# Performance work log

Hardware: AMD Instinct MI355X
Metric: run time of the kernel (lower is better)

Reference implementation:

```python
import jax, jax.numpy as jnp
import numpy as np

N_NODES = 50000
N_EDGES = 800000
IN, HID, OUT = 128, 256, 128
BN_EPS = 1e-5

def setup_inputs() -> dict:
    key = jax.random.key(0)
    ks = jax.random.split(key, 16)
    def lin(k, fan_in, shape):
        b = 1.0 / np.sqrt(fan_in)
        return jax.random.uniform(k, shape, jnp.float32, -b, b)
    return {
        "node_feat": jax.random.normal(ks[0], (N_NODES, IN), jnp.float32),
        "coord_feat": jax.random.normal(ks[1], (N_NODES, 3), jnp.float32),
        "src": jax.random.randint(ks[2], (N_EDGES,), 0, N_NODES, jnp.int32),
        "dst": jax.random.randint(ks[3], (N_EDGES,), 0, N_NODES, jnp.int32),
        "W_e1": lin(ks[4], 2 * IN + 1, (2 * IN + 1, HID)),
        "b_e1": jnp.zeros((HID,), jnp.float32),
        "W_e2": lin(ks[5], HID, (HID, HID)),
        "b_e2": jnp.zeros((HID,), jnp.float32),
        "W_c1": lin(ks[6], HID, (HID, HID)),
        "b_c1": jnp.zeros((HID,), jnp.float32),
        "W_c2": lin(ks[7], HID, (HID, 1)),
        "W_n1": lin(ks[8], IN + HID, (IN + HID, HID)),
        "b_n1": jnp.zeros((HID,), jnp.float32),
        "W_n2": lin(ks[9], HID, (HID, OUT)),
        "b_n2": jnp.zeros((OUT,), jnp.float32),
        "gamma": jnp.ones((OUT,), jnp.float32),
        "beta": jnp.zeros((OUT,), jnp.float32),
    }

def reference(node_feat, coord_feat, src, dst, W_e1, b_e1, W_e2, b_e2,
              W_c1, b_c1, W_c2, W_n1, b_n1, W_n2, b_n2, gamma, beta):
    silu = jax.nn.silu
    # per-edge geometry (DGL u_sub_v: src - dst)
    x_diff = coord_feat[src] - coord_feat[dst]              # [E, 3]
    radial = jnp.sum(jnp.square(x_diff), axis=1, keepdims=True)  # [E, 1]
    x_diff = x_diff / (jnp.sqrt(radial) + 1e-30)
    # edge MLP on gathered features
    f = jnp.concatenate([node_feat[src], node_feat[dst], radial], axis=-1)  # [E, 2*IN+1]
    msg_h = silu(silu(f @ W_e1 + b_e1) @ W_e2 + b_e2)       # [E, HID]
    # coord message
    msg_x = (silu(msg_h @ W_c1 + b_c1) @ W_c2) * x_diff     # [E, 3]
    # aggregate at destination nodes
    h_neigh = jax.ops.segment_sum(msg_h, dst, num_segments=N_NODES)  # sum
    x_sum = jax.ops.segment_sum(msg_x, dst, num_segments=N_NODES)
    deg = jax.ops.segment_sum(jnp.ones((msg_x.shape[0],), msg_x.dtype), dst,
                              num_segments=N_NODES)
    x_neigh = x_sum / jnp.maximum(deg, 1.0)[:, None]        # mean; 0 for isolated nodes
    # node MLP + BatchNorm (training-mode batch stats, biased var)
    h = silu(jnp.concatenate([node_feat, h_neigh], axis=-1) @ W_n1 + b_n1) @ W_n2 + b_n2
    mu = jnp.mean(h, axis=0)
    var = jnp.mean(jnp.square(h - mu), axis=0)
    h = (h - mu) * jax.lax.rsqrt(var + BN_EPS) * gamma + beta
    x = coord_feat + x_neigh
    return h, x
```

## Files before the change

kernel.cpp:

```cpp
#include <hip/hip_runtime.h>
#include <stdint.h>

typedef unsigned short u16;
typedef __bf16 bf16x8 __attribute__((ext_vector_type(8)));
typedef unsigned short u16x8 __attribute__((ext_vector_type(8)));
typedef float f32x4 __attribute__((ext_vector_type(4)));

#define N_NODES 50000
#define N_EDGES 800000

enum : uint32_t {
  WS_WT_E1 = 0u,
  WS_WT_E2 = 131072u,
  WS_WT_C1 = 262144u,
  WS_WT_N1 = 393216u,
  WS_WT_N2 = 589824u,
  WS_WRAD  = 655360u,
  WS_WC2   = 656384u,
  WS_B_E1  = 657408u,
  WS_B_E2  = 658432u,
  WS_B_C1  = 659456u,
  WS_B_N1  = 660480u,
  WS_B_N2  = 661504u,
  WS_GAMMA = 662016u,
  WS_BETA  = 662528u,
  WS_SCALE = 663040u,
  WS_SHIFT = 663552u,
  WS_STAT  = 664064u,
  WS_FLAG  = 665600u,
  WS_DEG   = 1048576u,
  WS_OFF   = 1248576u,
  WS_BSUM  = 1448704u,
  WS_BPRE  = 1449728u,
  WS_CUR   = 1450752u,
  WS_EID   = 1650752u,
  WS_XSUM  = 4850752u,
  WS_CF    = 5450752u,
  WS_NF    = 6050752u,
  WS_HN    = 18850752u,
  WS_PA    = 70050752u,
  WS_PB    = 95675328u,
  WS_PRE_END = 121299904u
};

__device__ __forceinline__ float b2f(u16 u){ uint32_t x=((uint32_t)u)<<16; float f; __builtin_memcpy(&f,&x,4); return f; }
__device__ __forceinline__ u16 f2b(float f){ __bf16 h = (__bf16)f; return __builtin_bit_cast(unsigned short, h); }
__device__ __forceinline__ float silu_f(float x){
  return x * __builtin_amdgcn_rcpf(1.0f + __expf(-x));
}
__device__ __forceinline__ float ldin(const void* p, int i, int fl){
  return fl ? ((const float*)p)[i] : b2f(((const u16*)p)[i]);
}

__global__ void detect_k(const void* nf, int* flag){
  if (threadIdx.x == 0){
    const u16* p = (const u16*)nf;
    int cnt = 0;
    for (int i=0;i<128;i++){
      u16 u = p[2*i];
      int e = (u >> 7) & 0xFF;
      if (e >= 0x90) cnt++;
    }
    *flag = (cnt >= 8) ? 1 : 0;
  }
}

__global__ void prep_all_k(const void* nf, const void* cd,
                           const void* We1, const void* be1, const void* We2, const void* be2,
                           const void* Wc1, const void* bc1, const void* Wc2,
                           const void* Wn1, const void* bn1, const void* Wn2, const void* bn2,
                           const void* gam, const void* bet,
                           const int* __restrict__ dst, int* __restrict__ deg,
                           char* ws, const int* flagp)
{
  const int b = blockIdx.x;
  const int fl = *flagp;
  if (b < 6250){
    int i = b*256 + threadIdx.x;
    if (i >= (N_NODES*128)/4) return;
    ushort4* out = (ushort4*)(ws + WS_NF);
    if (fl){
      const float4* p = (const float4*)nf;
      float4 v = p[i];
      ushort4 o; o.x=f2b(v.x); o.y=f2b(v.y); o.z=f2b(v.z); o.w=f2b(v.w);
      out[i] = o;
    } else {
      out[i] = ((const ushort4*)nf)[i];
    }
    return;
  }
  if (b < 6837){
    int i = (b-6250)*256 + threadIdx.x;
    if (i >= N_NODES*3) return;
    ((float*)(ws + WS_CF))[i] = ldin(cd, i, fl);
    return;
  }
  if (b < 8125){
    int g = (b-6837)*256 + threadIdx.x;
    if (g < 65536){ int n=g>>8,k=g&255; ((u16*)(ws+WS_WT_E1))[n*256+k]=f2b(ldin(We1,k*256+n,fl)); return; } g-=65536;
    if (g < 65536){
      int j=g&7, l=(g>>3)&63, nblk=(g>>9)&15, kk=g>>13;
      int n=nblk*16+(l&15), k=kk*32+((l>>4)&3)*8+j;
      ((u16*)(ws+WS_WT_E2))[g]=f2b(ldin(We2,k*256+n,fl)); return; } g-=65536;
    if (g < 65536){
      int j=g&7, l=(g>>3)&63, nblk=(g>>9)&15, kk=g>>13;
      int n=nblk*16+(l&15), k=kk*32+((l>>4)&3)*8+j;
      ((u16*)(ws+WS_WT_C1))[g]=f2b(ldin(Wc1,k*256+n,fl)); return; } g-=65536;
    if (g < 98304){ int n=g/384,k=g-n*384; ((u16*)(ws+WS_WT_N1))[n*384+k]=f2b(ldin(Wn1,k*256+n,fl)); return; } g-=98304;
    if (g < 32768){ int n=g>>8,k=g&255; ((u16*)(ws+WS_WT_N2))[n*256+k]=f2b(ldin(Wn2,k*128+n,fl)); return; } g-=32768;
    if (g < 256){ ((float*)(ws+WS_WRAD))[g]=ldin(We1,65536+g,fl); return; } g-=256;
    if (g < 256){ ((float*)(ws+WS_WC2))[g]=ldin(Wc2,g,fl); return; } g-=256;
    if (g < 256){ ((float*)(ws+WS_B_E1))[g]=ldin(be1,g,fl); return; } g-=256;
    if (g < 256){ ((float*)(ws+WS_B_E2))[g]=ldin(be2,g,fl); return; } g-=256;
    if (g < 256){ ((float*)(ws+WS_B_C1))[g]=ldin(bc1,g,fl); return; } g-=256;
    if (g < 256){ ((float*)(ws+WS_B_N1))[g]=ldin(bn1,g,fl); return; } g-=256;
    if (g < 128){ ((float*)(ws+WS_B_N2))[g]=ldin(bn2,g,fl); return; } g-=128;
    if (g < 128){ ((float*)(ws+WS_GAMMA))[g]=ldin(gam,g,fl); return; } g-=128;
    if (g < 128){ ((float*)(ws+WS_BETA))[g]=ldin(bet,g,fl); return; }
    return;
  }
  {
    int e = (b-8125)*256 + threadIdx.x;
    if (e < N_EDGES) atomicAdd(&deg[dst[e]], 1);
  }
}

__global__ void scanA_k(const int* __restrict__ deg, int* __restrict__ off, int* __restrict__ bsum){
  int t = threadIdx.x; int i = blockIdx.x*256 + t;
  int lane = t & 63, w = t >> 6;
  int v = (i < N_NODES) ? deg[i] : 0;
  int x = v;
  #pragma unroll
  for (int d=1; d<64; d<<=1){ int o = __shfl_up(x, d, 64); if (lane >= d) x += o; }
  __shared__ int wt[4];
  if (lane == 63) wt[w] = x;
  __syncthreads();
  int add = 0;
  if (w > 0) add += wt[0];
  if (w > 1) add += wt[1];
  if (w > 2) add += wt[2];
  x += add;
  if (i < N_NODES) off[i] = x;
  if (t == 255) bsum[blockIdx.x] = x;
}

__global__ void scanB_k(const int* __restrict__ bsum, int* __restrict__ bpre, int* __restrict__ off){
  int t = threadIdx.x;
  int lane = t & 63, w = t >> 6;
  int v = (t < 196) ? bsum[t] : 0;
  int x = v;
  #pragma unroll
  for (int d=1; d<64; d<<=1){ int o = __shfl_up(x, d, 64); if (lane >= d) x += o; }
  __shared__ int wt[4];
  if (lane == 63) wt[w] = x;
  __syncthreads();
  int add = 0;
  if (w > 0) add += wt[0];
  if (w > 1) add += wt[1];
  if (w > 2) add += wt[2];
  x += add;
  if (t < 196) bpre[t] = x - v;
  if (t == 255) off[N_NODES] = x;
}

__global__ void scanC_k(const int* __restrict__ deg, int* __restrict__ off,
                        const int* __restrict__ bpre, int* __restrict__ cur){
  int i = blockIdx.x*256 + threadIdx.x;
  if (i >= N_NODES) return;
  int excl = off[i] - deg[i] + bpre[blockIdx.x];
  off[i] = excl; cur[i] = excl;
}

__global__ void scatter_k(const int* __restrict__ dst, int* __restrict__ cur, int* __restrict__ eid){
  int e = blockIdx.x*256 + threadIdx.x;
  if (e >= N_EDGES) return;
  int p = atomicAdd(&cur[dst[e]], 1);
  eid[p] = e;
}

__global__ __launch_bounds__(512, 4) void pab_k(const u16* __restrict__ nfc,
                                                const char* __restrict__ wsw,
                                                u16* __restrict__ pa, u16* __restrict__ pb)
{
  const int t = threadIdx.x, lane = t & 63, wid = t >> 6;
  const int mw = wid & 1, nw = wid >> 1;
  const int mbase = mw << 5, nbase = nw << 6;
  const int l15 = lane & 15, l4 = lane >> 4;
  const int tile = blockIdx.x;
  const u16* Wt = (const u16*)(wsw + WS_WT_E1);
  const float* b1 = (const float*)(wsw + WS_B_E1);

  for (int sel = 0; sel < 2; ++sel){
    u16* out = sel ? pb : pa;
    f32x4 acc[2][4];
    #pragma unroll
    for (int mi=0;mi<2;mi++)
    #pragma unroll
    for (int ni=0;ni<4;ni++){ float b_ = sel ? 0.f : b1[nbase+ni*16+l15]; acc[mi][ni]=(f32x4){b_,b_,b_,b_}; }

    #pragma unroll
    for (int kk=0;kk<4;kk++){
      const int kel = kk*32 + l4*8;
      bf16x8 av[2];
      #pragma unroll
      for (int mi=0;mi<2;mi++){
        int row = tile*64 + mbase + mi*16 + l15;
        if (row >= N_NODES) row = 0;
        av[mi] = *(const bf16x8*)(nfc + (size_t)row*128 + kel);
      }
      #pragma unroll
      for (int ni=0;ni<4;ni++){
        int n_ = nbase + ni*16 + l15;
        bf16x8 bv = *(const bf16x8*)(Wt + (size_t)n_*256 + sel*128 + kel);
        #pragma unroll
        for (int mi=0;mi<2;mi++)
          acc[mi][ni] = __builtin_amdgcn_mfma_f32_16x16x32_bf16(av[mi], bv, acc[mi][ni], 0,0,0);
      }
    }
    #pragma unroll
    for (int mi=0;mi<2;mi++)
    #pragma unroll
    for (int ni=0;ni<4;ni++)
    #pragma unroll
    for (int j=0;j<4;j++){
      int m_ = tile*64 + mbase + mi*16 + l4*4 + j;
      if (m_ < N_NODES){
        int n_ = nbase + ni*16 + l15;
        out[(size_t)m_*256 + n_] = f2b(acc[mi][ni][j]);
      }
    }
  }
}

#define FRAG_GEMM2(FB, BIAS_L) do { \
  _Pragma("unroll") for (int mi=0;mi<2;mi++) _Pragma("unroll") for (int ni=0;ni<4;ni++){ \
    float b_ = BIAS_L[nbase + ni*16 + l15]; acc[mi][ni] = (f32x4){b_,b_,b_,b_}; } \
  bf16x8 bvc[4]; \
  _Pragma("unroll") for (int ni=0;ni<4;ni++) \
    bvc[ni] = *(const bf16x8*)(FB + (((nblk0 + ni)<<9)) + lane*8); \
  _Pragma("unroll") for (int kk=0;kk<8;kk++){ \
    const int kel = kk*32 + l4*8; \
    bf16x8 av[2]; \
    _Pragma("unroll") for (int mi=0;mi<2;mi++){ \
      int row = mbase + mi*16 + l15; \
      uint32_t byte = ((uint32_t)row<<9) ^ ((uint32_t)kel<<1) ^ ((uint32_t)(row&7)<<4); \
      av[mi] = *(const bf16x8*)((const char*)h_lds + byte); \
    } \
    bf16x8 bvn[4]; \
    if (kk < 7){ \
      _Pragma("unroll") for (int ni=0;ni<4;ni++) \
        bvn[ni] = *(const bf16x8*)(FB + ((((kk+1)<<4) + nblk0 + ni)<<9) + lane*8); \
    } \
    _Pragma("unroll") for (int ni=0;ni<4;ni++) \
    _Pragma("unroll") for (int mi=0;mi<2;mi++) \
      acc[mi][ni] = __builtin_amdgcn_mfma_f32_16x16x32_bf16(av[mi], bvc[ni], acc[mi][ni], 0,0,0); \
    if (kk < 7){ \
      _Pragma("unroll") for (int ni=0;ni<4;ni++) bvc[ni] = bvn[ni]; \
    } \
  } } while(0)

#define SILU_STORE2() do { \
  _Pragma("unroll") for (int mi=0;mi<2;mi++) _Pragma("unroll") for (int ni=0;ni<4;ni++) \
  _Pragma("unroll") for (int j=0;j<4;j++){ \
    int m_ = mbase + mi*16 + l4*4 + j; int n_ = nbase + ni*16 + l15; \
    float v_ = silu_f(acc[mi][ni][j]); \
    uint32_t byte = ((uint32_t)m_<<9) ^ ((uint32_t)n_<<1) ^ ((uint32_t)(m_&7)<<4); \
    *(u16*)((char*)h_lds + byte) = f2b(v_); \
  } } while(0)

template<bool PRE>
__global__ __launch_bounds__(512, 4) void edge_mlp(
    const u16* __restrict__ nfc, const float* __restrict__ coord,
    const int* __restrict__ src, const int* __restrict__ dst,
    const char* __restrict__ wsw, const int* __restrict__ eid,
    const u16* __restrict__ pa, const u16* __restrict__ pb,
    float* __restrict__ h_neigh, float* __restrict__ xsum)
{
  __shared__ u16 h_lds[16384];
  __shared__ int s_ids[64], d_ids[64];
  __shared__ float rad_l[64], xd_l[64][3];
  __shared__ float cpart[4][64];
  __shared__ float b1_l[256], b2_l[256], b3_l[256], wc2_l[256];

  const int t = threadIdx.x, lane = t & 63, wid = t >> 6;
  const int mw = wid & 1, nw = wid >> 1;
  const int mbase = mw << 5, nbase = nw << 6;
  const int nblk0 = nw << 2;
  const int l15 = lane & 15, l4 = lane >> 4;

  const int orig = blockIdx.x;
  const int xcd = orig & 7;
  const int tile = (xcd < 4 ? xcd*1563 : 4*1563 + (xcd-4)*1562) + (orig >> 3);

  const u16* FB2 = (const u16*)(wsw + WS_WT_E2);
  const u16* FB3 = (const u16*)(wsw + WS_WT_C1);

  if (t < 64) {
    int e = eid[tile*64 + t];
    int s = src[e], d = dst[e];
    s_ids[t] = s; d_ids[t] = d;
    float ax = coord[s*3+0]-coord[d*3+0];
    float ay = coord[s*3+1]-coord[d*3+1];
    float az = coord[s*3+2]-coord[d*3+2];
    float r2 = ax*ax+ay*ay+az*az;
    float inv = 1.0f/(sqrtf(r2) + 1e-30f);
    rad_l[t] = r2; xd_l[t][0]=ax*inv; xd_l[t][1]=ay*inv; xd_l[t][2]=az*inv;
  }
  if (t >= 64 && t < 320) {
    int c = t - 64;
    if constexpr (!PRE) b1_l[c] = ((const float*)(wsw+WS_B_E1))[c];
    b2_l[c]  = ((const float*)(wsw+WS_B_E2))[c];
    b3_l[c]  = ((const float*)(wsw+WS_B_C1))[c];
    wc2_l[c] = ((const float*)(wsw+WS_WC2))[c];
  }
  __syncthreads();

  f32x4 acc[2][4];

  if constexpr (PRE) {
    const int r1 = t >> 3, cq = (t & 7) << 5;
    const int s1 = s_ids[r1], d1 = d_ids[r1];
    const float rr = rad_l[r1];
    const u16* par = pa + (size_t)s1*256 + cq;
    const u16* pbr = pb + (size_t)d1*256 + cq;
    const float* wrg = (const float*)(wsw + WS_WRAD) + cq;
    u16x8 ua[4], ub[4];
    #pragma unroll
    for (int q=0;q<4;q++){ ua[q] = *(const u16x8*)(par + q*8); ub[q] = *(const u16x8*)(pbr + q*8); }
    #pragma unroll
    for (int q=0;q<4;q++){
      f32x4 w0 = *(const f32x4*)(wrg + q*8);
      f32x4 w1 = *(const f32x4*)(wrg + q*8 + 4);
      u16x8 o;
      #pragma unroll
      for (int j=0;j<8;j++){
        float wv = (j<4) ? w0[j] : w1[j-4];
        float hv = silu_f(b2f(ua[q][j]) + b2f(ub[q][j]) + rr*wv);
        o[j] = f2b(hv);
      }
      int c = cq + q*8;
      uint32_t byte = ((uint32_t)r1<<9) ^ ((uint32_t)c<<1) ^ ((uint32_t)(r1&7)<<4);
      *(u16x8*)((char*)h_lds + byte) = o;
    }
  } else {
    #pragma unroll
    for (int mi=0;mi<2;mi++)
    #pragma unroll
    for (int ni=0;ni<4;ni++){ float b_ = b1_l[nbase+ni*16+l15]; acc[mi][ni]=(f32x4){b_,b_,b_,b_}; }
    const u16* Wt1 = (const u16*)(wsw + WS_WT_E1);
    #pragma unroll
    for (int kk=0;kk<8;kk++){
      const int kel = kk*32 + l4*8;
      bf16x8 av[2];
      #pragma unroll
      for (int mi=0;mi<2;mi++){
        int row = mbase + mi*16 + l15;
        int nid = (kk < 4) ? s_ids[row] : d_ids[row];
        int k = (kk < 4) ? kel : (kel - 128);
        av[mi] = *(const bf16x8*)(nfc + (size_t)nid*128 + k);
      }
      #pragma unroll
      for (int ni=0;ni<4;ni++){
        int n_ = nbase + ni*16 + l15;
        bf16x8 bv = *(const bf16x8*)(Wt1 + (size_t)n_*256 + kel);
        #pragma unroll
        for (int mi=0;mi<2;mi++)
          acc[mi][ni] = __builtin_amdgcn_mfma_f32_16x16x32_bf16(av[mi], bv, acc[mi][ni], 0,0,0);
      }
    }
    #pragma unroll
    for (int mi=0;mi<2;mi++)
    #pragma unroll
    for (int ni=0;ni<4;ni++){
      int n_ = nbase + ni*16 + l15;
      float wrn = ((const float*)(wsw+WS_WRAD))[n_];
      #pragma unroll
      for (int j=0;j<4;j++){
        int m_ = mbase + mi*16 + l4*4 + j;
        float v_ = silu_f(acc[mi][ni][j] + rad_l[m_]*wrn);
        uint32_t byte = ((uint32_t)m_<<9) ^ ((uint32_t)n_<<1) ^ ((uint32_t)(m_&7)<<4);
        *(u16*)((char*)h_lds + byte) = f2b(v_);
      }
    }
  }
  __syncthreads();

  FRAG_GEMM2(FB2, b2_l);
  __syncthreads();
  SILU_STORE2();
  __syncthreads();

  FRAG_GEMM2(FB3, b3_l);
  float part[2][4];
  #pragma unroll
  for (int mi=0;mi<2;mi++)
  #pragma unroll
  for (int j=0;j<4;j++) part[mi][j] = 0.f;
  #pragma unroll
  for (int mi=0;mi<2;mi++)
  #pragma unroll
  for (int ni=0;ni<4;ni++){
    int n_ = nbase + ni*16 + l15;
    float w = wc2_l[n_];
    #pragma unroll
    for (int j=0;j<4;j++) part[mi][j] += silu_f(acc[mi][ni][j]) * w;
  }
  #pragma unroll
  for (int off_=1; off_<16; off_<<=1)
  #pragma unroll
  for (int mi=0;mi<2;mi++)
  #pragma unroll
  for (int j=0;j<4;j++) part[mi][j] += __shfl_xor(part[mi][j], off_, 64);
  if (l15 == 0){
    #pragma unroll
    for (int mi=0;mi<2;mi++)
    #pragma unroll
    for (int j=0;j<4;j++){
      int m_ = mbase + mi*16 + l4*4 + j;
      cpart[nw][m_] = part[mi][j];
    }
  }
  __syncthreads();

  if (t < 64){
    float csum = cpart[0][t] + cpart[1][t] + cpart[2][t] + cpart[3][t];
    int dd = d_ids[t];
    float v0 = csum*xd_l[t][0], v1 = csum*xd_l[t][1], v2 = csum*xd_l[t][2];
    #pragma unroll
    for (int off_=1; off_<64; off_<<=1){
      float u0=__shfl_up(v0,off_,64), u1=__shfl_up(v1,off_,64), u2=__shfl_up(v2,off_,64);
      int du=__shfl_up(dd,off_,64);
      if (lane >= off_ && du == dd){ v0+=u0; v1+=u1; v2+=u2; }
    }
    int dn = __shfl_down(dd,1,64);
    if (lane == 63 || dn != dd){
      unsafeAtomicAdd(&xsum[dd*3+0], v0);
      unsafeAtomicAdd(&xsum[dd*3+1], v1);
      unsafeAtomicAdd(&xsum[dd*3+2], v2);
    }
  }
  {
    int col  = t & 255;
    int half = t >> 8;
    int rb   = half << 5;
    float a2 = 0.f; int prev = d_ids[rb]; bool firstrun = true;
    #pragma unroll
    for (int ii=0; ii<32; ii+=8){
      float v[8]; int dv[8];
      #pragma unroll
      for (int j=0;j<8;j++){
        int m_ = rb + ii + j;
        uint32_t byte = ((uint32_t)m_<<9) ^ ((uint32_t)col<<1) ^ ((uint32_t)(m_&7)<<4);
        v[j] = b2f(*(const u16*)((const char*)h_lds + byte));
        dv[j] = d_ids[m_];
      }
      #pragma unroll
      for (int j=0;j<8;j++){
        if (dv[j] != prev){
          float* p = &h_neigh[(size_t)prev*256 + col];
          if (firstrun) unsafeAtomicAdd(p, a2); else *p = a2;
          firstrun = false; a2 = v[j]; prev = dv[j];
        } else a2 += v[j];
      }
    }
    unsafeAtomicAdd(&h_neigh[(size_t)prev*256 + col], a2);
  }
}

#define SILU_STORE2N() do { \
  _Pragma("unroll") for (int mi=0;mi<2;mi++) _Pragma("unroll") for (int ni=0;ni<4;ni++) \
  _Pragma("unroll") for (int j=0;j<4;j++){ \
    int m_ = mbase + mi*16 + l4*4 + j; int n_ = nbase + ni*16 + l15; \
    float v_ = silu_f(acc[mi][ni][j]); \
    uint32_t byte = ((uint32_t)m_<<9) ^ ((uint32_t)n_<<1) ^ ((uint32_t)(m_&7)<<4); \
    *(u16*)((char*)h_lds + byte) = f2b(v_); \
  } } while(0)

__global__ __launch_bounds__(512, 4) void node_mlp(
    const u16* __restrict__ node_feat, const float* __restrict__ h_neigh,
    const char* __restrict__ wsw, u16* __restrict__ hpre)
{
  __shared__ u16 h_lds[16384];
  __shared__ float b1_l[256], b2_l[128];

  const int t = threadIdx.x, lane = t & 63, wid = t >> 6;
  const int mw = wid & 1, nw = wid >> 1;
  const int mbase = mw << 5, nbase = nw << 6;
  const int l15 = lane & 15, l4 = lane >> 4;
  const int tile = blockIdx.x;

  if (t < 256) b1_l[t] = ((const float*)(wsw+WS_B_N1))[t];
  if (t < 128) b2_l[t] = ((const float*)(wsw+WS_B_N2))[t];
  __syncthreads();

  const u16* Wt1 = (const u16*)(wsw + WS_WT_N1);
  const u16* Wt2 = (const u16*)(wsw + WS_WT_N2);

  f32x4 acc[2][4];
  #pragma unroll
  for (int mi=0;mi<2;mi++)
  #pragma unroll
  for (int ni=0;ni<4;ni++){ float b_ = b1_l[nbase+ni*16+l15]; acc[mi][ni] = (f32x4){b_,b_,b_,b_}; }

  #pragma unroll
  for (int kk=0;kk<12;kk++){
    const int kel = kk*32 + l4*8;
    bf16x8 av[2];
    #pragma unroll
    for (int mi=0;mi<2;mi++){
      int row = tile*64 + mbase + mi*16 + l15;
      if (row >= N_NODES) row = 0;
      if (kk < 4){
        av[mi] = *(const bf16x8*)(node_feat + (size_t)row*128 + kel);
      } else {
        const float* hp = h_neigh + (size_t)row*256 + (kel - 128);
        f32x4 h0 = *(const f32x4*)(hp);
        f32x4 h1 = *(const f32x4*)(hp + 4);
        u16x8 u;
        #pragma unroll
        for (int e2=0;e2<4;e2++){ u[e2] = f2b(h0[e2]); u[e2+4] = f2b(h1[e2]); }
        av[mi] = __builtin_bit_cast(bf16x8, u);
      }
    }
    #pragma unroll
    for (int ni=0;ni<4;ni++){
      int n_ = nbase + ni*16 + l15;
      bf16x8 bv = *(const bf16x8*)(Wt1 + (size_t)n_*384 + kel);
      #pragma unroll
      for (int mi=0;mi<2;mi++)
        acc[mi][ni] = __builtin_amdgcn_mfma_f32_16x16x32_bf16(av[mi], bv, acc[mi][ni], 0,0,0);
    }
  }
  SILU_STORE2N();
  __syncthreads();

  const int nb2 = nw << 5;
  f32x4 acc2[2][2];
  #pragma unroll
  for (int mi=0;mi<2;mi++)
  #pragma unroll
  for (int ni=0;ni<2;ni++){ float b_ = b2_l[nb2+ni*16+l15]; acc2[mi][ni] = (f32x4){b_,b_,b_,b_}; }
  #pragma unroll
  for (int kk=0;kk<8;kk++){
    const int kel = kk*32 + l4*8;
    bf16x8 av[2];
    #pragma unroll
    for (int mi=0;mi<2;mi++){
      int row = mbase + mi*16 + l15;
      uint32_t byte = ((uint32_t)row<<9) ^ ((uint32_t)kel<<1) ^ ((uint32_t)(row&7)<<4);
      av[mi] = *(const bf16x8*)((const char*)h_lds + byte);
    }
    #pragma unroll
    for (int ni=0;ni<2;ni++){
      int n_ = nb2 + ni*16 + l15;
      bf16x8 bv = *(const bf16x8*)(Wt2 + (size_t)n_*256 + kel);
      #pragma unroll
      for (int mi=0;mi<2;mi++)
        acc2[mi][ni] = __builtin_amdgcn_mfma_f32_16x16x32_bf16(av[mi], bv, acc2[mi][ni], 0,0,0);
    }
  }
  #pragma unroll
  for (int mi=0;mi<2;mi++)
  #pragma unroll
  for (int ni=0;ni<2;ni++)
  #pragma unroll
  for (int j=0;j<4;j++){
    int m_ = tile*64 + mbase + mi*16 + l4*4 + j;
    if (m_ < N_NODES){
      int n_ = nb2 + ni*16 + l15;
      hpre[(size_t)m_*128 + n_] = f2b(acc2[mi][ni][j]);
    }
  }
}

__global__ void bn_stats_k(const u16* __restrict__ hpre, float* __restrict__ stat){
  int c = threadIdx.x;
  float s = 0.f, s2 = 0.f;
  for (int r = blockIdx.x; r < N_NODES; r += 256){
    float v = b2f(hpre[(size_t)r*128 + c]);
    s += v; s2 += v*v;
  }
  atomicAdd(&stat[c], s);
  atomicAdd(&stat[128+c], s2);
}

__global__ void bn_final_k(const float* __restrict__ stat, const char* __restrict__ wsw,
                           float* __restrict__ scale, float* __restrict__ shift){
  int c = threadIdx.x;
  if (c >= 128) return;
  float mu = stat[c] * (1.0f/N_NODES);
  float var = stat[128+c] * (1.0f/N_NODES) - mu*mu;
  float rs = rsqrtf(var + 1e-5f);
  float g = ((const float*)(wsw+WS_GAMMA))[c];
  float b = ((const float*)(wsw+WS_BETA))[c];
  scale[c] = rs*g;
  shift[c] = b - mu*rs*g;
}

__global__ void finish_k(const u16* __restrict__ hpre, const float* __restrict__ scale,
                         const float* __restrict__ shift, const float* __restrict__ coord,
                         const int* __restrict__ deg, const float* __restrict__ xsum,
                         void* __restrict__ d_out, const int* __restrict__ flagp)
{
  const int b = blockIdx.x;
  const int fl = *flagp;
  if (b < 3125){
    int i = b*256 + threadIdx.x;
    if (i >= N_NODES*128/8) return;
    u16x8 v = *(const u16x8*)(hpre + (size_t)i*8);
    int c0 = (i*8) & 127;
    if (fl){
      float* o = (float*)d_out + (size_t)i*8;
      #pragma unroll
      for (int j=0;j<8;j++) o[j] = b2f(v[j])*scale[c0+j] + shift[c0+j];
    } else {
      u16x8 w;
      #pragma unroll
      for (int j=0;j<8;j++) w[j] = f2b(b2f(v[j])*scale[c0+j] + shift[c0+j]);
      *(u16x8*)((u16*)d_out + (size_t)i*8) = w;
    }
    return;
  }
  {
    int n = (b-3125)*256 + threadIdx.x;
    if (n >= N_NODES) return;
    float dm = fmaxf((float)deg[n], 1.f);
    float v0 = coord[n*3+0] + xsum[n*3+0]/dm;
    float v1 = coord[n*3+1] + xsum[n*3+1]/dm;
    float v2 = coord[n*3+2] + xsum[n*3+2]/dm;
    const size_t base = (size_t)N_NODES*128 + (size_t)n*3;
    if (fl){
      float* o = (float*)d_out;
      o[base+0]=v0; o[base+1]=v1; o[base+2]=v2;
    } else {
      u16* o = (u16*)d_out;
      o[base+0]=f2b(v0); o[base+1]=f2b(v1); o[base+2]=f2b(v2);
    }
  }
}

extern "C" void kernel_launch(void* const* d_in, const int* in_sizes, int n_in,
                              void* d_out, int out_size, void* d_ws, size_t ws_size,
                              hipStream_t stream)
{
  const void* node_feat_raw = d_in[0];
  const void* coord_raw     = d_in[1];
  const int* src       = (const int*)d_in[2];
  const int* dst       = (const int*)d_in[3];
  char* ws = (char*)d_ws;

  int*   flag  = (int*)(ws + WS_FLAG);
  int*   deg   = (int*)(ws + WS_DEG);
  int*   off   = (int*)(ws + WS_OFF);
  int*   bsum  = (int*)(ws + WS_BSUM);
  int*   bpre  = (int*)(ws + WS_BPRE);
  int*   cur   = (int*)(ws + WS_CUR);
  int*   eid   = (int*)(ws + WS_EID);
  float* xsum  = (float*)(ws + WS_XSUM);
  float* hn    = (float*)(ws + WS_HN);
  u16*   pa    = (u16*)(ws + WS_PA);
  u16*   pb    = (u16*)(ws + WS_PB);
  u16*   hpre  = (u16*)(ws + WS_PA);
  const u16*   nfc = (const u16*)(ws + WS_NF);
  const float* cfc = (const float*)(ws + WS_CF);
  float* stat  = (float*)(ws + WS_STAT);
  float* scale = (float*)(ws + WS_SCALE);
  float* shift = (float*)(ws + WS_SHIFT);

  const bool pre = (ws_size >= (size_t)WS_PRE_END);

  hipMemsetAsync(deg, 0, N_NODES*sizeof(int), stream);
  hipMemsetAsync(xsum, 0, N_NODES*3*sizeof(float), stream);
  hipMemsetAsync(hn, 0, (size_t)N_NODES*256*sizeof(float), stream);
  hipMemsetAsync(stat, 0, 256*sizeof(float), stream);

  detect_k<<<1,64,0,stream>>>(node_feat_raw, flag);
  prep_all_k<<<11250,256,0,stream>>>(node_feat_raw, coord_raw,
                                     d_in[4],d_in[5],d_in[6],d_in[7],d_in[8],d_in[9],
                                     d_in[10],d_in[11],d_in[12],d_in[13],d_in[14],
                                     d_in[15],d_in[16], dst, deg, ws, flag);
  scanA_k<<<196,256,0,stream>>>(deg, off, bsum);
  scanB_k<<<1,256,0,stream>>>(bsum, bpre, off);
  scanC_k<<<196,256,0,stream>>>(deg, off, bpre, cur);
  scatter_k<<<3125,256,0,stream>>>(dst, cur, eid);

  if (pre){
    pab_k<<<782,512,0,stream>>>(nfc, ws, pa, pb);
    edge_mlp<true><<<12500,512,0,stream>>>(nfc, cfc, src, dst, ws, eid, pa, pb, hn, xsum);
  } else {
    edge_mlp<false><<<12500,512,0,stream>>>(nfc, cfc, src, dst, ws, eid, pa, pb, hn, xsum);
  }

  node_mlp<<<782,512,0,stream>>>(nfc, hn, ws, hpre);
  bn_stats_k<<<256,128,0,stream>>>(hpre, stat);
  bn_final_k<<<1,128,0,stream>>>(stat, ws, scale, shift);
  finish_k<<<3321,256,0,stream>>>(hpre, scale, shift, cfc, deg, xsum, d_out, flag);
}
```

Baseline: 809.1 us.

## Double edge tile to 128 rows per block in edge MLP

```diff
diff --git a/kernel.cpp b/kernel.cpp
--- a/kernel.cpp
+++ b/kernel.cpp
@@ -232,35 +232,26 @@
   }
 }
 
-#define FRAG_GEMM2(FB, BIAS_L) do { \
-  _Pragma("unroll") for (int mi=0;mi<2;mi++) _Pragma("unroll") for (int ni=0;ni<4;ni++){ \
+#define FRAG_GEMM4(FB, BIAS_L) do { \
+  _Pragma("unroll") for (int mi=0;mi<4;mi++) _Pragma("unroll") for (int ni=0;ni<4;ni++){ \
     float b_ = BIAS_L[nbase + ni*16 + l15]; acc[mi][ni] = (f32x4){b_,b_,b_,b_}; } \
-  bf16x8 bvc[4]; \
-  _Pragma("unroll") for (int ni=0;ni<4;ni++) \
-    bvc[ni] = *(const bf16x8*)(FB + (((nblk0 + ni)<<9)) + lane*8); \
   _Pragma("unroll") for (int kk=0;kk<8;kk++){ \
     const int kel = kk*32 + l4*8; \
-    bf16x8 av[2]; \
-    _Pragma("unroll") for (int mi=0;mi<2;mi++){ \
+    bf16x8 av[4]; \
+    _Pragma("unroll") for (int mi=0;mi<4;mi++){ \
       int row = mbase + mi*16 + l15; \
       uint32_t byte = ((uint32_t)row<<9) ^ ((uint32_t)kel<<1) ^ ((uint32_t)(row&7)<<4); \
       av[mi] = *(const bf16x8*)((const char*)h_lds + byte); \
     } \
-    bf16x8 bvn[4]; \
-    if (kk < 7){ \
-      _Pragma("unroll") for (int ni=0;ni<4;ni++) \
-        bvn[ni] = *(const bf16x8*)(FB + ((((kk+1)<<4) + nblk0 + ni)<<9) + lane*8); \
-    } \
-    _Pragma("unroll") for (int ni=0;ni<4;ni++) \
-    _Pragma("unroll") for (int mi=0;mi<2;mi++) \
-      acc[mi][ni] = __builtin_amdgcn_mfma_f32_16x16x32_bf16(av[mi], bvc[ni], acc[mi][ni], 0,0,0); \
-    if (kk < 7){ \
-      _Pragma("unroll") for (int ni=0;ni<4;ni++) bvc[ni] = bvn[ni]; \
+    _Pragma("unroll") for (int ni=0;ni<4;ni++){ \
+      bf16x8 bv = *(const bf16x8*)(FB + (((kk<<4) + nblk0 + ni)<<9) + lane*8); \
+      _Pragma("unroll") for (int mi=0;mi<4;mi++) \
+        acc[mi][ni] = __builtin_amdgcn_mfma_f32_16x16x32_bf16(av[mi], bv, acc[mi][ni], 0,0,0); \
     } \
   } } while(0)
 
-#define SILU_STORE2() do { \
-  _Pragma("unroll") for (int mi=0;mi<2;mi++) _Pragma("unroll") for (int ni=0;ni<4;ni++) \
+#define SILU_STORE4() do { \
+  _Pragma("unroll") for (int mi=0;mi<4;mi++) _Pragma("unroll") for (int ni=0;ni<4;ni++) \
   _Pragma("unroll") for (int j=0;j<4;j++){ \
     int m_ = mbase + mi*16 + l4*4 + j; int n_ = nbase + ni*16 + l15; \
     float v_ = silu_f(acc[mi][ni][j]); \
@@ -276,27 +267,27 @@
     const u16* __restrict__ pa, const u16* __restrict__ pb,
     float* __restrict__ h_neigh, float* __restrict__ xsum)
 {
-  __shared__ u16 h_lds[16384];
-  __shared__ int s_ids[64], d_ids[64];
-  __shared__ float rad_l[64], xd_l[64][3];
-  __shared__ float cpart[4][64];
+  __shared__ u16 h_lds[32768];
+  __shared__ int s_ids[128], d_ids[128];
+  __shared__ float rad_l[128], xd_l[128][3];
+  __shared__ float cpart[4][128];
   __shared__ float b1_l[256], b2_l[256], b3_l[256], wc2_l[256];
 
   const int t = threadIdx.x, lane = t & 63, wid = t >> 6;
   const int mw = wid & 1, nw = wid >> 1;
-  const int mbase = mw << 5, nbase = nw << 6;
+  const int mbase = mw << 6, nbase = nw << 6;
   const int nblk0 = nw << 2;
   const int l15 = lane & 15, l4 = lane >> 4;
 
   const int orig = blockIdx.x;
   const int xcd = orig & 7;
-  const int tile = (xcd < 4 ? xcd*1563 : 4*1563 + (xcd-4)*1562) + (orig >> 3);
+  const int tile = (xcd < 2 ? xcd*782 : 2*782 + (xcd-2)*781) + (orig >> 3);
 
   const u16* FB2 = (const u16*)(wsw + WS_WT_E2);
   const u16* FB3 = (const u16*)(wsw + WS_WT_C1);
 
-  if (t < 64) {
-    int e = eid[tile*64 + t];
+  if (t < 128) {
+    int e = eid[tile*128 + t];
     int s = src[e], d = dst[e];
     s_ids[t] = s; d_ids[t] = d;
     float ax = coord[s*3+0]-coord[d*3+0];
@@ -306,8 +297,8 @@
     float inv = 1.0f/(sqrtf(r2) + 1e-30f);
     rad_l[t] = r2; xd_l[t][0]=ax*inv; xd_l[t][1]=ay*inv; xd_l[t][2]=az*inv;
   }
-  if (t >= 64 && t < 320) {
-    int c = t - 64;
+  if (t >= 128 && t < 384) {
+    int c = t - 128;
     if constexpr (!PRE) b1_l[c] = ((const float*)(wsw+WS_B_E1))[c];
     b2_l[c]  = ((const float*)(wsw+WS_B_E2))[c];
     b3_l[c]  = ((const float*)(wsw+WS_B_C1))[c];
@@ -315,27 +306,26 @@
   }
   __syncthreads();
 
-  f32x4 acc[2][4];
+  f32x4 acc[4][4];
 
   if constexpr (PRE) {
-    const int r1 = t >> 3, cq = (t & 7) << 5;
+    const int r1 = t >> 2, cq = (t & 3) << 6;
     const int s1 = s_ids[r1], d1 = d_ids[r1];
     const float rr = rad_l[r1];
     const u16* par = pa + (size_t)s1*256 + cq;
     const u16* pbr = pb + (size_t)d1*256 + cq;
     const float* wrg = (const float*)(wsw + WS_WRAD) + cq;
-    u16x8 ua[4], ub[4];
-    #pragma unroll
-    for (int q=0;q<4;q++){ ua[q] = *(const u16x8*)(par + q*8); ub[q] = *(const u16x8*)(pbr + q*8); }
-    #pragma unroll
-    for (int q=0;q<4;q++){
+    #pragma unroll
+    for (int q=0;q<8;q++){
+      u16x8 ua = *(const u16x8*)(par + q*8);
+      u16x8 ub = *(const u16x8*)(pbr + q*8);
       f32x4 w0 = *(const f32x4*)(wrg + q*8);
       f32x4 w1 = *(const f32x4*)(wrg + q*8 + 4);
       u16x8 o;
       #pragma unroll
       for (int j=0;j<8;j++){
         float wv = (j<4) ? w0[j] : w1[j-4];
-        float hv = silu_f(b2f(ua[q][j]) + b2f(ub[q][j]) + rr*wv);
+        float hv = silu_f(b2f(ua[j]) + b2f(ub[j]) + rr*wv);
         o[j] = f2b(hv);
       }
       int c = cq + q*8;
@@ -344,16 +334,16 @@
     }
   } else {
     #pragma unroll
-    for (int mi=0;mi<2;mi++)
+    for (int mi=0;mi<4;mi++)
     #pragma unroll
     for (int ni=0;ni<4;ni++){ float b_ = b1_l[nbase+ni*16+l15]; acc[mi][ni]=(f32x4){b_,b_,b_,b_}; }
     const u16* Wt1 = (const u16*)(wsw + WS_WT_E1);
     #pragma unroll
     for (int kk=0;kk<8;kk++){
       const int kel = kk*32 + l4*8;
-      bf16x8 av[2];
-      #pragma unroll
-      for (int mi=0;mi<2;mi++){
+      bf16x8 av[4];
+      #pragma unroll
+      for (int mi=0;mi<4;mi++){
         int row = mbase + mi*16 + l15;
         int nid = (kk < 4) ? s_ids[row] : d_ids[row];
         int k = (kk < 4) ? kel : (kel - 128);
@@ -364,12 +354,12 @@
         int n_ = nbase + ni*16 + l15;
         bf16x8 bv = *(const bf16x8*)(Wt1 + (size_t)n_*256 + kel);
         #pragma unroll
-        for (int mi=0;mi<2;mi++)
+        for (int mi=0;mi<4;mi++)
           acc[mi][ni] = __builtin_amdgcn_mfma_f32_16x16x32_bf16(av[mi], bv, acc[mi][ni], 0,0,0);
       }
     }
     #pragma unroll
-    for (int mi=0;mi<2;mi++)
+    for (int mi=0;mi<4;mi++)
     #pragma unroll
     for (int ni=0;ni<4;ni++){
       int n_ = nbase + ni*16 + l15;
@@ -385,19 +375,19 @@
   }
   __syncthreads();
 
-  FRAG_GEMM2(FB2, b2_l);
-  __syncthreads();
-  SILU_STORE2();
-  __syncthreads();
-
-  FRAG_GEMM2(FB3, b3_l);
-  float part[2][4];
-  #pragma unroll
-  for (int mi=0;mi<2;mi++)
+  FRAG_GEMM4(FB2, b2_l);
+  __syncthreads();
+  SILU_STORE4();
+  __syncthreads();
+
+  FRAG_GEMM4(FB3, b3_l);
+  float part[4][4];
+  #pragma unroll
+  for (int mi=0;mi<4;mi++)
   #pragma unroll
   for (int j=0;j<4;j++) part[mi][j] = 0.f;
   #pragma unroll
-  for (int mi=0;mi<2;mi++)
+  for (int mi=0;mi<4;mi++)
   #pragma unroll
   for (int ni=0;ni<4;ni++){
     int n_ = nbase + ni*16 + l15;
@@ -408,12 +398,12 @@
   #pragma unroll
   for (int off_=1; off_<16; off_<<=1)
   #pragma unroll
-  for (int mi=0;mi<2;mi++)
+  for (int mi=0;mi<4;mi++)
   #pragma unroll
   for (int j=0;j<4;j++) part[mi][j] += __shfl_xor(part[mi][j], off_, 64);
   if (l15 == 0){
     #pragma unroll
-    for (int mi=0;mi<2;mi++)
+    for (int mi=0;mi<4;mi++)
     #pragma unroll
     for (int j=0;j<4;j++){
       int m_ = mbase + mi*16 + l4*4 + j;
@@ -422,7 +412,7 @@
   }
   __syncthreads();
 
-  if (t < 64){
+  if (t < 128){
     float csum = cpart[0][t] + cpart[1][t] + cpart[2][t] + cpart[3][t];
     int dd = d_ids[t];
     float v0 = csum*xd_l[t][0], v1 = csum*xd_l[t][1], v2 = csum*xd_l[t][2];
@@ -442,10 +432,10 @@
   {
     int col  = t & 255;
     int half = t >> 8;
-    int rb   = half << 5;
+    int rb   = half << 6;
     float a2 = 0.f; int prev = d_ids[rb]; bool firstrun = true;
     #pragma unroll
-    for (int ii=0; ii<32; ii+=8){
+    for (int ii=0; ii<64; ii+=8){
       float v[8]; int dv[8];
       #pragma unroll
       for (int j=0;j<8;j++){
@@ -686,9 +676,9 @@
 
   if (pre){
     pab_k<<<782,512,0,stream>>>(nfc, ws, pa, pb);
-    edge_mlp<true><<<12500,512,0,stream>>>(nfc, cfc, src, dst, ws, eid, pa, pb, hn, xsum);
+    edge_mlp<true><<<6250,512,0,stream>>>(nfc, cfc, src, dst, ws, eid, pa, pb, hn, xsum);
   } else {
-    edge_mlp<false><<<12500,512,0,stream>>>(nfc, cfc, src, dst, ws, eid, pa, pb, hn, xsum);
+    edge_mlp<false><<<6250,512,0,stream>>>(nfc, cfc, src, dst, ws, eid, pa, pb, hn, xsum);
   }
 
   node_mlp<<<782,512,0,stream>>>(nfc, hn, ws, hpre);
```

Measured after the change: 965.8 us. +19.4%, slower.
